# Kernel optimization log

Measured on AMD Instinct MI355X. Metric: run time of the kernel, lower is better.

Reference implementation:

```python
import jax, jax.numpy as jnp
import numpy as np

N = 50000
E = 800000
C = 64


def setup_inputs() -> dict:
    key = jax.random.key(0)
    ks = jax.random.split(key, 16)
    s = 0.05
    x = jax.random.normal(ks[0], (N, C), jnp.float32)
    edge_attr = jax.random.uniform(ks[1], (E, 4), dtype=jnp.float32)
    edge_index = jax.random.randint(ks[2], (2, E), 0, N)
    deg_hist = jax.random.uniform(ks[3], (N,), dtype=jnp.float32) * 32.0
    W = jax.random.normal(ks[4], (C, C), jnp.float32) * s          # self.weight[0]
    We = jax.random.normal(ks[5], (3, C), jnp.float32) * s         # edge_encoder
    be = jnp.zeros((C,), jnp.float32)
    Wpre = jax.random.normal(ks[6], (3 * C, C), jnp.float32) * s   # pre_nn Linear
    bpre = jnp.zeros((C,), jnp.float32)
    A_S = 4 * 3  # aggregators * scalers
    Wpost = jax.random.normal(ks[7], ((A_S + 1) * C, C), jnp.float32) * s
    bpost = jnp.zeros((C,), jnp.float32)
    Wih = jax.random.normal(ks[8], (C, 3 * C), jnp.float32) * s    # GRUCell input weights (transposed)
    bih = jnp.zeros((3 * C,), jnp.float32)
    Whh = jax.random.normal(ks[9], (C, 3 * C), jnp.float32) * s    # GRUCell hidden weights (transposed)
    bhh = jnp.zeros((3 * C,), jnp.float32)
    return dict(x=x, edge_attr=edge_attr, deg_hist=deg_hist, W=W, We=We, be=be,
                Wpre=Wpre, bpre=bpre, Wpost=Wpost, bpost=bpost,
                Wih=Wih, bih=bih, Whh=Whh, bhh=bhh, edge_index=edge_index)


def reference(x, edge_attr, deg_hist, W, We, be, Wpre, bpre, Wpost, bpost,
              Wih, bih, Whh, bhh, edge_index):
    n_nodes = x.shape[0]
    # gated path: m = x @ weight[0]
    m = x @ W  # [N, C]
    src, dst = edge_index[0], edge_index[1]
    # message: edge-weight scaling + edge encoder + pre-MLP (single Linear)
    ew = edge_attr[:, 3:4]                         # [E, 1]
    ea = edge_attr[:, :3] @ We + be                # [E, C]
    xi = ew * m[dst]                               # x_i (target)
    xj = ew * m[src]                               # x_j (source)
    ea = ew * ea
    h = jnp.concatenate([xi, xj, ea], axis=-1) @ Wpre + bpre  # [E, C]
    # multi-aggregator scatter: mean, min, max, std (keyed by target node)
    ones = jnp.ones((h.shape[0],), h.dtype)
    cnt = jax.ops.segment_sum(ones, dst, num_segments=n_nodes)       # [N]
    safe = jnp.maximum(cnt, 1.0)[:, None]
    s1 = jax.ops.segment_sum(h, dst, num_segments=n_nodes)
    s2 = jax.ops.segment_sum(h * h, dst, num_segments=n_nodes)
    mean = s1 / safe
    mean_sq = s2 / safe
    std = jnp.sqrt(jax.nn.relu(mean_sq - mean * mean) + 1e-5)
    has = (cnt > 0)[:, None]
    mn = jnp.where(has, jax.ops.segment_min(h, dst, num_segments=n_nodes), 0.0)
    mx = jnp.where(has, jax.ops.segment_max(h, dst, num_segments=n_nodes), 0.0)
    agg = jnp.concatenate([mean, mn, mx, std], axis=-1)  # [N, 4C]
    # degree scalers (faithfully replicating the cumulative reassignment in the torch loop)
    deg = jnp.maximum(cnt, 1.0)[:, None]
    avg_log = jnp.mean(jnp.log(deg_hist + 1.0))
    logd = jnp.log(deg + 1.0)
    o1 = agg                          # identity
    o2 = o1 * (logd / avg_log)        # amplification
    o3 = o2 * (avg_log / logd)        # attenuation applied on top of o2 (torch bug, kept)
    out = jnp.concatenate([o1, o2, o3], axis=-1)          # [N, 12C]
    # post-MLP on cat([m, aggregated])
    out = jnp.concatenate([m, out], axis=-1) @ Wpost + bpost  # [N, C]
    # GRUCell(out, x): torch gate order r, z, n
    gi = out @ Wih + bih
    gh = x @ Whh + bhh
    ir, iz, i_n = jnp.split(gi, 3, axis=-1)
    hr, hz, h_n = jnp.split(gh, 3, axis=-1)
    r = jax.nn.sigmoid(ir + hr)
    z = jax.nn.sigmoid(iz + hz)
    n = jnp.tanh(i_n + r * h_n)
    return (1.0 - z) * n + z * x
```

## Files before the change

### kernel.cpp

```cpp
#include <hip/hip_runtime.h>
#include <math.h>

#define NN  50000
#define NNP 50048
#define NE  800000
#define REP 16

#define B_BG1   0u
#define B_BG2A  49152u
#define B_BG2B  90112u
#define B_BG3   122880u
#define B_WE2   147456u
#define B_BE2   148224u
#define B_B3    148480u
#define B_SUML  149248u
#define B_XB    149504u
#define B_NF    6555648u
#define B_GH    19367936u
#define B_A2    38586368u
#define B_S2F   70617088u
#define B_CNT   70817280u
#define B_OFFS  74017280u
#define B_RANK  74217344u
#define B_ROFF  77417344u
#define B_EL2   80617344u
#define B_PART  87017344u

#define SCAN_B  196

typedef __attribute__((ext_vector_type(8))) short s8v;
typedef __attribute__((ext_vector_type(4))) short s4v;
typedef __attribute__((ext_vector_type(4))) float f4v;

__device__ inline short f2b(float f){
    union { float f; unsigned u; } v; v.f = f;
    unsigned r = v.u + 0x7fffu + ((v.u >> 16) & 1u);
    return (short)(r >> 16);
}
__device__ inline float b2f(short b){
    union { unsigned u; float f; } v; v.u = ((unsigned)(unsigned short)b) << 16;
    return v.f;
}

__global__ __launch_bounds__(256) void k_prep(const float* __restrict__ x,
    const float* __restrict__ dh, const int* __restrict__ dstA,
    const float* __restrict__ W, const float* __restrict__ Wpre,
    const float* __restrict__ We, const float* __restrict__ be,
    const float* __restrict__ bpost, const float* __restrict__ Wpost,
    const float* __restrict__ Wih, const float* __restrict__ bih,
    const float* __restrict__ Whh, int* __restrict__ cnt,
    int* __restrict__ rank, unsigned char* __restrict__ wsb)
{
    __shared__ float sred[4];
    int b = blockIdx.x, t = threadIdx.x;
    {
        int e = b * 256 + t;
        int r = b & (REP - 1);
        rank[e] = atomicAdd(&cnt[r * NN + dstA[e]], 1);
    }

    if (b < 38) {
        int idx = b * 256 + t;
        if (idx < 3072) {
            short* dst = (short*)(wsb + B_BG1);
            int lane = idx & 63, ts = idx >> 6;
            int tt = ts >> 1, s = ts & 1;
            int quad = lane >> 4, l15 = lane & 15, n = tt*16 + l15;
            for (int j = 0; j < 8; ++j) {
                int k = s*32 + quad*8 + j;
                float v;
                if (n < 64)       v = W[k*64 + n];
                else if (n < 128) { v = 0.f; for (int c = 0; c < 64; ++c) v += W[k*64+c]*Wpre[c*64 + (n-64)]; }
                else if (n < 192) { v = 0.f; for (int c = 0; c < 64; ++c) v += W[k*64+c]*Wpre[4096 + c*64 + (n-128)]; }
                else              v = Whh[k*192 + (n-192)];
                dst[((size_t)ts*64 + lane)*8 + j] = f2b(v);
            }
        } else if (idx < 5632) {
            int id = idx - 3072;
            short* dst = (short*)(wsb + B_BG2A);
            int lane = id & 63, ts = id >> 6;
            int quad = lane >> 4, l15 = lane & 15;
            int tt = ts / 10, s = ts % 10;
            int n = tt*16 + l15;
            for (int j = 0; j < 8; ++j) {
                int k = s*32 + quad*8 + j;
                float v;
                if (k < 64) v = Wpost[k*64 + n];
                else {
                    int kk = k - 64, ch = kk >> 2, st = kk & 3;
                    int ok = 64 + st*64 + ch;
                    v = Wpost[ok*64 + n] + Wpost[(ok + 512)*64 + n];
                }
                dst[((size_t)ts*64 + lane)*8 + j] = f2b(v);
            }
        } else if (idx < 7680) {
            int id = idx - 5632;
            short* dst = (short*)(wsb + B_BG2B);
            int lane = id & 63, ts = id >> 6;
            int quad = lane >> 4, l15 = lane & 15;
            int tt = ts / 8, s = ts % 8;
            int n = tt*16 + l15;
            for (int j = 0; j < 8; ++j) {
                int k = s*32 + quad*8 + j;
                int ch = k >> 2, st = k & 3;
                int ok = 320 + st*64 + ch;
                dst[((size_t)ts*64 + lane)*8 + j] = f2b(Wpost[ok*64 + n]);
            }
        } else if (idx < 9216) {
            int id = idx - 7680;
            short* dst = (short*)(wsb + B_BG3);
            int lane = id & 63, ts = id >> 6;
            int tt = ts >> 1, s = ts & 1;
            int quad = lane >> 4, l15 = lane & 15, n = tt*16 + l15;
            for (int j = 0; j < 8; ++j) {
                int k = s*32 + quad*8 + j;
                dst[((size_t)ts*64 + lane)*8 + j] = f2b(Wih[k*192 + n]);
            }
        } else if (idx < 9408) {
            int t2 = idx - 9216; int kk = t2 >> 6, j = t2 & 63;
            float v = 0.f;
            for (int c = 0; c < 64; ++c) v += We[kk*64 + c] * Wpre[(128+c)*64 + j];
            ((float*)(wsb + B_WE2))[t2] = v;
        } else if (idx < 9472) {
            int j = idx - 9408;
            float v = 0.f;
            for (int c = 0; c < 64; ++c) v += be[c] * Wpre[(128+c)*64 + j];
            ((float*)(wsb + B_BE2))[j] = v;
        } else if (idx < 9664) {
            int j = idx - 9472;
            float v = bih[j];
            for (int k = 0; k < 64; ++k) v += bpost[k] * Wih[k*192 + j];
            ((float*)(wsb + B_B3))[j] = v;
        }
    } else if (b < 1601) {
        int i = (b - 38) * 256 + t;
        if (i < 400000) {
            const float4* xp = (const float4*)(x + (size_t)i * 8);
            float4 p0 = xp[0], p1 = xp[1];
            s8v o;
            o[0]=f2b(p0.x); o[1]=f2b(p0.y); o[2]=f2b(p0.z); o[3]=f2b(p0.w);
            o[4]=f2b(p1.x); o[5]=f2b(p1.y); o[6]=f2b(p1.z); o[7]=f2b(p1.w);
            *(s8v*)((short*)(wsb + B_XB) + (size_t)i * 8) = o;
        }
    } else if (b < 1797) {
        int i = (b - 1601) * 256 + t;
        float v = (i < NN) ? logf(dh[i] + 1.f) : 0.f;
        #pragma unroll
        for (int m = 32; m >= 1; m >>= 1) v += __shfl_xor(v, m, 64);
        if ((t & 63) == 0) sred[t >> 6] = v;
        __syncthreads();
        if (t == 0) atomicAdd((float*)(wsb + B_SUML), sred[0]+sred[1]+sred[2]+sred[3]);
    }
}

__global__ __launch_bounds__(256) void k_scanA(const int* __restrict__ cnt,
    int* __restrict__ offs, int* __restrict__ roff, int* __restrict__ part)
{
    __shared__ int sh[256];
    int t = threadIdx.x, i = blockIdx.x * 256 + t;
    int v = 0;
    int pre[REP];
    if (i < NN) {
        #pragma unroll
        for (int r = 0; r < REP; ++r) {
            pre[r] = v;
            v += cnt[r * NN + i];
        }
    }
    sh[t] = v; __syncthreads();
    #pragma unroll
    for (int o = 1; o < 256; o <<= 1) {
        int u = (t >= o) ? sh[t - o] : 0;
        __syncthreads();
        sh[t] += u;
        __syncthreads();
    }
    if (i < NN) {
        offs[i] = sh[t] - v;
        int4* rp = (int4*)(roff + (size_t)i * REP);
        #pragma unroll
        for (int q = 0; q < REP/4; ++q)
            rp[q] = make_int4(pre[q*4], pre[q*4+1], pre[q*4+2], pre[q*4+3]);
    }
    if (t == 255) part[blockIdx.x] = sh[255];
}

__global__ __launch_bounds__(256) void k_scanC(const int* __restrict__ part,
    int* __restrict__ offs, int* __restrict__ roff)
{
    __shared__ int sh[256];
    int b = blockIdx.x, t = threadIdx.x;
    int v = (t < SCAN_B) ? part[t] : 0;
    sh[t] = v; __syncthreads();
    #pragma unroll
    for (int o = 1; o < 256; o <<= 1) {
        int u = (t >= o) ? sh[t - o] : 0;
        __syncthreads();
        sh[t] += u;
        __syncthreads();
    }
    int base = (b == 0) ? 0 : sh[b - 1];
    int i = b * 256 + t;
    if (i < NN) {
        int fo = offs[i] + base;
        offs[i] = fo;
        int4* rp = (int4*)(roff + (size_t)i * REP);
        #pragma unroll
        for (int q = 0; q < REP/4; ++q) {
            int4 r4 = rp[q];
            r4.x += fo; r4.y += fo; r4.z += fo; r4.w += fo;
            rp[q] = r4;
        }
    }
    if (b == 0 && t == 0) offs[NN] = NE;
}

__global__ __launch_bounds__(256) void k_scatter(const int* __restrict__ srcA,
    const int* __restrict__ dstA, const int* __restrict__ rank,
    const int* __restrict__ roff, int2* __restrict__ el2)
{
    int e = blockIdx.x * 256 + threadIdx.x;
    int r = blockIdx.x & (REP - 1);
    int dst = dstA[e];
    int p = roff[dst * REP + r] + rank[e];
    el2[p] = make_int2(e, srcA[e]);
}

__global__ __launch_bounds__(256) void k_g1(unsigned char* __restrict__ wsb)
{
    const short* xb = (const short*)(wsb + B_XB);
    const short* bf = (const short*)(wsb + B_BG1);
    short* a2 = (short*)(wsb + B_A2);
    short* nf = (short*)(wsb + B_NF);
    short* gh = (short*)(wsb + B_GH);
    int w = threadIdx.x >> 6, lane = threadIdx.x & 63;
    int quad = lane >> 4, l15 = lane & 15;
    int R0 = blockIdx.x * 64 + w * 16;
    const short* arow = xb + (size_t)(R0 + l15) * 64 + quad * 8;
    s8v a0 = *(const s8v*)(arow);
    s8v a1 = *(const s8v*)(arow + 32);
    f4v acc[24];
    #pragma unroll
    for (int t = 0; t < 24; ++t) acc[t] = (f4v){0.f,0.f,0.f,0.f};
    #pragma unroll
    for (int t = 0; t < 24; ++t) {
        s8v b0 = *(const s8v*)(bf + ((size_t)(t*2+0)*64 + lane)*8);
        s8v b1 = *(const s8v*)(bf + ((size_t)(t*2+1)*64 + lane)*8);
        acc[t] = __builtin_amdgcn_mfma_f32_16x16x32_bf16(a0, b0, acc[t], 0, 0, 0);
        acc[t] = __builtin_amdgcn_mfma_f32_16x16x32_bf16(a1, b1, acc[t], 0, 0, 0);
    }
    #pragma unroll
    for (int t = 0; t < 24; ++t) {
        #pragma unroll
        for (int r = 0; r < 4; ++r) {
            int row = R0 + quad*4 + r;
            if (row >= NN) continue;
            short v = f2b(acc[t][r]);
            if (t < 4)       a2[(size_t)row*320 + t*16 + l15] = v;
            else if (t < 12) nf[(size_t)row*128 + (t-4)*16 + l15] = v;
            else             gh[(size_t)row*192 + (t-12)*16 + l15] = v;
        }
    }
}

__global__ __launch_bounds__(256) void k_agg(const float* __restrict__ eattr,
    const float* __restrict__ bpre, unsigned char* __restrict__ wsb)
{
    __shared__ float4 sEA[4][64];
    __shared__ int    sOFF[4][64];
    int lane = threadIdx.x & 63;
    int w    = threadIdx.x >> 6;
    int wid  = blockIdx.x * 4 + w;
    const int* offs = (const int*)(wsb + B_OFFS);
    const int2* el2 = (const int2*)(wsb + B_EL2);
    const unsigned char* nfb = wsb + B_NF;
    const short* nf = (const short*)(wsb + B_NF);
    const float* we2p = (const float*)(wsb + B_WE2);
    float we0 = we2p[lane], we1 = we2p[64 + lane], we2v = we2p[128 + lane];
    float be2l = ((const float*)(wsb + B_BE2))[lane];
    float bprel = bpre[lane];
    float rcpavg = (float)NN / ((const float*)(wsb + B_SUML))[0];
    const float4* e4 = (const float4*)eattr;
    unsigned laneoff = 128u + 2u * (unsigned)lane;
    short* a2b = (short*)(wsb + B_A2);
    float* s2f = (float*)(wsb + B_S2F);

    for (int n = wid; n < NN; n += 8192) {
        float md2l = b2f(nf[(size_t)n * 128 + lane]);
        float tbase = md2l + be2l;
        int o0 = offs[n], o1e = offs[n + 1];
        float s = 0.f, ss = 0.f, mn = INFINITY, mx = -INFINITY;
        for (int base = o0; base < o1e; base += 64) {
            int cnt = o1e - base; if (cnt > 64) cnt = 64;
            if (lane < cnt) {
                int2 es = el2[base + lane];
                sOFF[w][lane] = es.y << 8;
                sEA[w][lane]  = e4[es.x];
            }
            for (int d0 = 0; d0 < cnt; d0 += 8) {
                float msv[8];
                #pragma unroll
                for (int u = 0; u < 8; ++u) {
                    int d = d0 + u; if (d > cnt - 1) d = cnt - 1;
                    unsigned off = (unsigned)sOFF[w][d] + laneoff;
                    msv[u] = b2f(*(const short*)(nfb + off));
                }
                #pragma unroll
                for (int u = 0; u < 8; ++u) {
                    int d = d0 + u;
                    if (d < cnt) {
                        float4 ea = sEA[w][d];
                        float t = tbase + msv[u];
                        t = fmaf(ea.x, we0, t);
                        t = fmaf(ea.y, we1, t);
                        t = fmaf(ea.z, we2v, t);
                        float h = fmaf(ea.w, t, bprel);
                        s += h; ss = fmaf(h, h, ss);
                        mn = fminf(mn, h); mx = fmaxf(mx, h);
                    }
                }
            }
        }
        int deg = o1e - o0;
        float safe = (float)(deg > 0 ? deg : 1);
        float mean = s / safe;
        float var  = ss / safe - mean * mean;
        float stdv = sqrtf(fmaxf(var, 0.f) + 1e-5f);
        if (deg == 0) { mn = 0.f; mx = 0.f; }
        s4v o; o[0] = f2b(mean); o[1] = f2b(mn); o[2] = f2b(mx); o[3] = f2b(stdv);
        *(s4v*)(a2b + (size_t)n * 320 + 64 + (lane << 2)) = o;
        if (lane == 0) s2f[n] = logf(safe + 1.f) * rcpavg;
    }
}

__global__ __launch_bounds__(256) void k_g23(const float* __restrict__ x,
    const float* __restrict__ bhh, unsigned char* __restrict__ wsb,
    float* __restrict__ out)
{
    __shared__ short sm[64 * 72];
    __shared__ float sS2[64];
    const short* a2  = (const short*)(wsb + B_A2);
    const short* bgA = (const short*)(wsb + B_BG2A);
    const short* bgB = (const short*)(wsb + B_BG2B);
    const short* bg3 = (const short*)(wsb + B_BG3);
    const short* gh  = (const short*)(wsb + B_GH);
    const float* b3  = (const float*)(wsb + B_B3);
    const float* s2f = (const float*)(wsb + B_S2F);
    int w = threadIdx.x >> 6, lane = threadIdx.x & 63;
    int quad = lane >> 4, l15 = lane & 15;
    int R0 = blockIdx.x * 64 + w * 16;

    {
        int i = threadIdx.x;
        if (i < 64) {
            int row = blockIdx.x * 64 + i;
            sS2[i] = (row < NN) ? s2f[row] : 0.f;
        }
    }

    const short* aBase = a2 + (size_t)(R0 + l15) * 320 + quad * 8;
    f4v acc1[4], acc2[4];
    #pragma unroll
    for (int t = 0; t < 4; ++t) { acc1[t] = (f4v){0.f,0.f,0.f,0.f}; acc2[t] = (f4v){0.f,0.f,0.f,0.f}; }
    #pragma unroll 2
    for (int s = 0; s < 10; ++s) {
        s8v a = *(const s8v*)(aBase + s * 32);
        #pragma unroll
        for (int t = 0; t < 4; ++t) {
            s8v b = *(const s8v*)(bgA + ((size_t)(t*10 + s)*64 + lane)*8);
            acc1[t] = __builtin_amdgcn_mfma_f32_16x16x32_bf16(a, b, acc1[t], 0, 0, 0);
        }
    }
    #pragma unroll 2
    for (int s = 0; s < 8; ++s) {
        s8v a = *(const s8v*)(aBase + 64 + s * 32);
        #pragma unroll
        for (int t = 0; t < 4; ++t) {
            s8v b = *(const s8v*)(bgB + ((size_t)(t*8 + s)*64 + lane)*8);
            acc2[t] = __builtin_amdgcn_mfma_f32_16x16x32_bf16(a, b, acc2[t], 0, 0, 0);
        }
    }
    __syncthreads();
    #pragma unroll
    for (int t = 0; t < 4; ++t)
        #pragma unroll
        for (int r = 0; r < 4; ++r) {
            int lr = w*16 + quad*4 + r;
            float v = acc1[t][r] + sS2[lr] * acc2[t][r];
            sm[lr * 72 + t*16 + l15] = f2b(v);
        }
    __syncthreads();

    const short* arow = sm + (w*16 + l15) * 72 + quad * 8;
    s8v a0 = *(const s8v*)(arow);
    s8v a1 = *(const s8v*)(arow + 32);
    f4v acc[12];
    #pragma unroll
    for (int t = 0; t < 12; ++t) acc[t] = (f4v){0.f,0.f,0.f,0.f};
    #pragma unroll
    for (int t = 0; t < 12; ++t) {
        s8v b0 = *(const s8v*)(bg3 + ((size_t)(t*2+0)*64 + lane)*8);
        s8v b1 = *(const s8v*)(bg3 + ((size_t)(t*2+1)*64 + lane)*8);
        acc[t] = __builtin_amdgcn_mfma_f32_16x16x32_bf16(a0, b0, acc[t], 0, 0, 0);
        acc[t] = __builtin_amdgcn_mfma_f32_16x16x32_bf16(a1, b1, acc[t], 0, 0, 0);
    }
    #pragma unroll
    for (int t = 0; t < 4; ++t) {
        #pragma unroll
        for (int r = 0; r < 4; ++r) {
            int row = R0 + quad*4 + r;
            if (row >= NN) continue;
            int c = t*16 + l15;
            float ir  = acc[t][r]   + b3[c];
            float iz  = acc[t+4][r] + b3[64 + c];
            float inn = acc[t+8][r] + b3[128 + c];
            const short* g = gh + (size_t)row * 192;
            float hr = b2f(g[c])       + bhh[c];
            float hz = b2f(g[64 + c])  + bhh[64 + c];
            float hn = b2f(g[128 + c]) + bhh[128 + c];
            float rr = 1.f / (1.f + expf(-(ir + hr)));
            float zz = 1.f / (1.f + expf(-(iz + hz)));
            float nn = tanhf(inn + rr * hn);
            out[(size_t)row*64 + c] = (1.f - zz)*nn + zz*x[(size_t)row*64 + c];
        }
    }
}

extern "C" void kernel_launch(void* const* d_in, const int* in_sizes, int n_in,
                              void* d_out, int out_size, void* d_ws, size_t ws_size,
                              hipStream_t stream)
{
    const float* x     = (const float*)d_in[0];
    const float* eattr = (const float*)d_in[1];
    const float* dh    = (const float*)d_in[2];
    const float* W     = (const float*)d_in[3];
    const float* We    = (const float*)d_in[4];
    const float* be    = (const float*)d_in[5];
    const float* Wpre  = (const float*)d_in[6];
    const float* bpre  = (const float*)d_in[7];
    const float* Wpost = (const float*)d_in[8];
    const float* bpost = (const float*)d_in[9];
    const float* Wih   = (const float*)d_in[10];
    const float* bih   = (const float*)d_in[11];
    const float* Whh   = (const float*)d_in[12];
    const float* bhh   = (const float*)d_in[13];
    const int*   eidx  = (const int*)d_in[14];
    unsigned char* wsb = (unsigned char*)d_ws;
    float* out = (float*)d_out;
    const int* srcA = eidx;
    const int* dstA = eidx + NE;
    int* cnt  = (int*)(wsb + B_CNT);
    int* offs = (int*)(wsb + B_OFFS);
    int* rank = (int*)(wsb + B_RANK);
    int* roff = (int*)(wsb + B_ROFF);
    int2* el2 = (int2*)(wsb + B_EL2);
    int* part = (int*)(wsb + B_PART);

    hipMemsetAsync(wsb + B_SUML, 0, 4, stream);
    hipMemsetAsync(cnt, 0, REP * NN * sizeof(int), stream);

    k_prep    <<<3125, 256, 0, stream>>>(x, dh, dstA, W, Wpre, We, be, bpost,
                                         Wpost, Wih, bih, Whh, cnt, rank, wsb);
    k_scanA   <<<SCAN_B, 256, 0, stream>>>(cnt, offs, roff, part);
    k_scanC   <<<SCAN_B, 256, 0, stream>>>(part, offs, roff);
    k_scatter <<<NE/256, 256, 0, stream>>>(srcA, dstA, rank, roff, el2);
    k_g1      <<<NNP/64, 256, 0, stream>>>(wsb);
    k_agg     <<<2048, 256, 0, stream>>>(eattr, bpre, wsb);
    k_g23     <<<NNP/64, 256, 0, stream>>>(x, bhh, wsb, out);
}
```

Baseline: 261.6 us.

## Fuse GRU hidden projection into final GEMM via stacked input/hidden weights

The x@Whh hidden-gate GEMM moves out of the first node GEMM, which no longer writes a bf16 gh buffer to workspace, and into the final kernel. There the GRU GEMM uses K=128 by concatenating the post-MLP output with bf16 x, with a block-structured weight that sums r/z contributions and keeps the n-gate hidden part separate. This removes the gh write and read (about 19 MB each way) and the per-element bias loads, at the cost of extra MFMAs, zero-padded weight blocks and more accumulator registers in k_g23.

New measurement: 310.0 us. +18.5%, slower.

```diff
diff --git a/kernel.cpp b/kernel.cpp
--- a/kernel.cpp
+++ b/kernel.cpp
@@ -7,24 +7,23 @@
 #define REP 16
 
 #define B_BG1   0u
-#define B_BG2A  49152u
-#define B_BG2B  90112u
-#define B_BG3   122880u
-#define B_WE2   147456u
-#define B_BE2   148224u
-#define B_B3    148480u
-#define B_SUML  149248u
-#define B_XB    149504u
-#define B_NF    6555648u
-#define B_GH    19367936u
-#define B_A2    38586368u
-#define B_S2F   70617088u
-#define B_CNT   70817280u
-#define B_OFFS  74017280u
-#define B_RANK  74217344u
-#define B_ROFF  77417344u
-#define B_EL2   80617344u
-#define B_PART  87017344u
+#define B_BG2A  24576u
+#define B_BG2B  65536u
+#define B_BG3   98304u
+#define B_WE2   163840u
+#define B_BE2   164608u
+#define B_B4    164864u
+#define B_SUML  165888u
+#define B_XB    166912u
+#define B_NF    6573056u
+#define B_A2    19385344u
+#define B_S2F   51416064u
+#define B_CNT   51616064u
+#define B_OFFS  54816064u
+#define B_RANK  55016072u
+#define B_ROFF  58216072u
+#define B_EL2   61416072u
+#define B_PART  67816072u
 
 #define SCAN_B  196
 
@@ -48,8 +47,9 @@
     const float* __restrict__ We, const float* __restrict__ be,
     const float* __restrict__ bpost, const float* __restrict__ Wpost,
     const float* __restrict__ Wih, const float* __restrict__ bih,
-    const float* __restrict__ Whh, int* __restrict__ cnt,
-    int* __restrict__ rank, unsigned char* __restrict__ wsb)
+    const float* __restrict__ Whh, const float* __restrict__ bhh,
+    int* __restrict__ cnt, int* __restrict__ rank,
+    unsigned char* __restrict__ wsb)
 {
     __shared__ float sred[4];
     int b = blockIdx.x, t = threadIdx.x;
@@ -59,27 +59,27 @@
         rank[e] = atomicAdd(&cnt[r * NN + dstA[e]], 1);
     }
 
-    if (b < 38) {
+    if (b < 42) {
         int idx = b * 256 + t;
-        if (idx < 3072) {
+        int lane = idx & 63;
+        int quad = lane >> 4, l15 = lane & 15;
+        if (idx < 1536) {
             short* dst = (short*)(wsb + B_BG1);
-            int lane = idx & 63, ts = idx >> 6;
+            int ts = idx >> 6;
             int tt = ts >> 1, s = ts & 1;
-            int quad = lane >> 4, l15 = lane & 15, n = tt*16 + l15;
+            int n = tt*16 + l15;
             for (int j = 0; j < 8; ++j) {
                 int k = s*32 + quad*8 + j;
                 float v;
                 if (n < 64)       v = W[k*64 + n];
                 else if (n < 128) { v = 0.f; for (int c = 0; c < 64; ++c) v += W[k*64+c]*Wpre[c*64 + (n-64)]; }
-                else if (n < 192) { v = 0.f; for (int c = 0; c < 64; ++c) v += W[k*64+c]*Wpre[4096 + c*64 + (n-128)]; }
-                else              v = Whh[k*192 + (n-192)];
+                else              { v = 0.f; for (int c = 0; c < 64; ++c) v += W[k*64+c]*Wpre[4096 + c*64 + (n-128)]; }
                 dst[((size_t)ts*64 + lane)*8 + j] = f2b(v);
             }
-        } else if (idx < 5632) {
-            int id = idx - 3072;
+        } else if (idx < 4096) {
+            int id = idx - 1536;
             short* dst = (short*)(wsb + B_BG2A);
-            int lane = id & 63, ts = id >> 6;
-            int quad = lane >> 4, l15 = lane & 15;
+            int ts = id >> 6;
             int tt = ts / 10, s = ts % 10;
             int n = tt*16 + l15;
             for (int j = 0; j < 8; ++j) {
@@ -93,11 +93,10 @@
                 }
                 dst[((size_t)ts*64 + lane)*8 + j] = f2b(v);
             }
-        } else if (idx < 7680) {
-            int id = idx - 5632;
+        } else if (idx < 6144) {
+            int id = idx - 4096;
             short* dst = (short*)(wsb + B_BG2B);
-            int lane = id & 63, ts = id >> 6;
-            int quad = lane >> 4, l15 = lane & 15;
+            int ts = id >> 6;
             int tt = ts / 8, s = ts % 8;
             int n = tt*16 + l15;
             for (int j = 0; j < 8; ++j) {
@@ -106,34 +105,46 @@
                 int ok = 320 + st*64 + ch;
                 dst[((size_t)ts*64 + lane)*8 + j] = f2b(Wpost[ok*64 + n]);
             }
-        } else if (idx < 9216) {
-            int id = idx - 7680;
+        } else if (idx < 10240) {
+            int id = idx - 6144;
             short* dst = (short*)(wsb + B_BG3);
-            int lane = id & 63, ts = id >> 6;
-            int tt = ts >> 1, s = ts & 1;
-            int quad = lane >> 4, l15 = lane & 15, n = tt*16 + l15;
+            int ts = id >> 6;
+            int tt = ts >> 2, s = ts & 3;
+            int n = tt*16 + l15;
             for (int j = 0; j < 8; ++j) {
                 int k = s*32 + quad*8 + j;
-                dst[((size_t)ts*64 + lane)*8 + j] = f2b(Wih[k*192 + n]);
-            }
-        } else if (idx < 9408) {
-            int t2 = idx - 9216; int kk = t2 >> 6, j = t2 & 63;
+                float v;
+                if (k < 64) v = (n < 192) ? Wih[k*192 + n] : 0.f;
+                else {
+                    int kk = k - 64;
+                    if (n < 128)      v = Whh[kk*192 + n];
+                    else if (n < 192) v = 0.f;
+                    else              v = Whh[kk*192 + 128 + (n - 192)];
+                }
+                dst[((size_t)ts*64 + lane)*8 + j] = f2b(v);
+            }
+        } else if (idx < 10432) {
+            int t2 = idx - 10240; int kk = t2 >> 6, j = t2 & 63;
             float v = 0.f;
             for (int c = 0; c < 64; ++c) v += We[kk*64 + c] * Wpre[(128+c)*64 + j];
             ((float*)(wsb + B_WE2))[t2] = v;
-        } else if (idx < 9472) {
-            int j = idx - 9408;
+        } else if (idx < 10496) {
+            int j = idx - 10432;
             float v = 0.f;
             for (int c = 0; c < 64; ++c) v += be[c] * Wpre[(128+c)*64 + j];
             ((float*)(wsb + B_BE2))[j] = v;
-        } else if (idx < 9664) {
-            int j = idx - 9472;
-            float v = bih[j];
-            for (int k = 0; k < 64; ++k) v += bpost[k] * Wih[k*192 + j];
-            ((float*)(wsb + B_B3))[j] = v;
-        }
-    } else if (b < 1601) {
-        int i = (b - 38) * 256 + t;
+        } else if (idx < 10752) {
+            int j = idx - 10496;
+            float v;
+            if (j < 192) {
+                v = bih[j];
+                for (int k = 0; k < 64; ++k) v += bpost[k] * Wih[k*192 + j];
+                if (j < 128) v += bhh[j];
+            } else v = bhh[128 + (j - 192)];
+            ((float*)(wsb + B_B4))[j] = v;
+        }
+    } else if (b < 1605) {
+        int i = (b - 42) * 256 + t;
         if (i < 400000) {
             const float4* xp = (const float4*)(x + (size_t)i * 8);
             float4 p0 = xp[0], p1 = xp[1];
@@ -142,8 +153,8 @@
             o[4]=f2b(p1.x); o[5]=f2b(p1.y); o[6]=f2b(p1.z); o[7]=f2b(p1.w);
             *(s8v*)((short*)(wsb + B_XB) + (size_t)i * 8) = o;
         }
-    } else if (b < 1797) {
-        int i = (b - 1601) * 256 + t;
+    } else if (b < 1801) {
+        int i = (b - 1605) * 256 + t;
         float v = (i < NN) ? logf(dh[i] + 1.f) : 0.f;
         #pragma unroll
         for (int m = 32; m >= 1; m >>= 1) v += __shfl_xor(v, m, 64);
@@ -162,10 +173,7 @@
     int pre[REP];
     if (i < NN) {
         #pragma unroll
-        for (int r = 0; r < REP; ++r) {
-            pre[r] = v;
-            v += cnt[r * NN + i];
-        }
+        for (int r = 0; r < REP; ++r) { pre[r] = v; v += cnt[r * NN + i]; }
     }
     sh[t] = v; __syncthreads();
     #pragma unroll
@@ -232,33 +240,31 @@
     const short* bf = (const short*)(wsb + B_BG1);
     short* a2 = (short*)(wsb + B_A2);
     short* nf = (short*)(wsb + B_NF);
-    short* gh = (short*)(wsb + B_GH);
     int w = threadIdx.x >> 6, lane = threadIdx.x & 63;
     int quad = lane >> 4, l15 = lane & 15;
     int R0 = blockIdx.x * 64 + w * 16;
     const short* arow = xb + (size_t)(R0 + l15) * 64 + quad * 8;
     s8v a0 = *(const s8v*)(arow);
     s8v a1 = *(const s8v*)(arow + 32);
-    f4v acc[24];
-    #pragma unroll
-    for (int t = 0; t < 24; ++t) acc[t] = (f4v){0.f,0.f,0.f,0.f};
-    #pragma unroll
-    for (int t = 0; t < 24; ++t) {
+    f4v acc[12];
+    #pragma unroll
+    for (int t = 0; t < 12; ++t) acc[t] = (f4v){0.f,0.f,0.f,0.f};
+    #pragma unroll
+    for (int t = 0; t < 12; ++t) {
         s8v b0 = *(const s8v*)(bf + ((size_t)(t*2+0)*64 + lane)*8);
         s8v b1 = *(const s8v*)(bf + ((size_t)(t*2+1)*64 + lane)*8);
         acc[t] = __builtin_amdgcn_mfma_f32_16x16x32_bf16(a0, b0, acc[t], 0, 0, 0);
         acc[t] = __builtin_amdgcn_mfma_f32_16x16x32_bf16(a1, b1, acc[t], 0, 0, 0);
     }
     #pragma unroll
-    for (int t = 0; t < 24; ++t) {
+    for (int t = 0; t < 12; ++t) {
         #pragma unroll
         for (int r = 0; r < 4; ++r) {
             int row = R0 + quad*4 + r;
             if (row >= NN) continue;
             short v = f2b(acc[t][r]);
-            if (t < 4)       a2[(size_t)row*320 + t*16 + l15] = v;
-            else if (t < 12) nf[(size_t)row*128 + (t-4)*16 + l15] = v;
-            else             gh[(size_t)row*192 + (t-12)*16 + l15] = v;
+            if (t < 4) a2[(size_t)row*320 + t*16 + l15] = v;
+            else       nf[(size_t)row*128 + (t-4)*16 + l15] = v;
         }
     }
 }
@@ -334,21 +340,24 @@
 }
 
 __global__ __launch_bounds__(256) void k_g23(const float* __restrict__ x,
-    const float* __restrict__ bhh, unsigned char* __restrict__ wsb,
-    float* __restrict__ out)
+    unsigned char* __restrict__ wsb, float* __restrict__ out)
 {
     __shared__ short sm[64 * 72];
     __shared__ float sS2[64];
     const short* a2  = (const short*)(wsb + B_A2);
+    const short* xb  = (const short*)(wsb + B_XB);
     const short* bgA = (const short*)(wsb + B_BG2A);
     const short* bgB = (const short*)(wsb + B_BG2B);
     const short* bg3 = (const short*)(wsb + B_BG3);
-    const short* gh  = (const short*)(wsb + B_GH);
-    const float* b3  = (const float*)(wsb + B_B3);
+    const float* b4  = (const float*)(wsb + B_B4);
     const float* s2f = (const float*)(wsb + B_S2F);
     int w = threadIdx.x >> 6, lane = threadIdx.x & 63;
     int quad = lane >> 4, l15 = lane & 15;
     int R0 = blockIdx.x * 64 + w * 16;
+
+    const short* xrow = xb + (size_t)(R0 + l15) * 64 + quad * 8;
+    s8v q0 = *(const s8v*)(xrow);
+    s8v q1 = *(const s8v*)(xrow + 32);
 
     {
         int i = threadIdx.x;
@@ -392,17 +401,21 @@
     __syncthreads();
 
     const short* arow = sm + (w*16 + l15) * 72 + quad * 8;
-    s8v a0 = *(const s8v*)(arow);
-    s8v a1 = *(const s8v*)(arow + 32);
-    f4v acc[12];
-    #pragma unroll
-    for (int t = 0; t < 12; ++t) acc[t] = (f4v){0.f,0.f,0.f,0.f};
-    #pragma unroll
-    for (int t = 0; t < 12; ++t) {
-        s8v b0 = *(const s8v*)(bg3 + ((size_t)(t*2+0)*64 + lane)*8);
-        s8v b1 = *(const s8v*)(bg3 + ((size_t)(t*2+1)*64 + lane)*8);
-        acc[t] = __builtin_amdgcn_mfma_f32_16x16x32_bf16(a0, b0, acc[t], 0, 0, 0);
-        acc[t] = __builtin_amdgcn_mfma_f32_16x16x32_bf16(a1, b1, acc[t], 0, 0, 0);
+    s8v p0 = *(const s8v*)(arow);
+    s8v p1 = *(const s8v*)(arow + 32);
+    f4v acc[16];
+    #pragma unroll
+    for (int t = 0; t < 16; ++t) acc[t] = (f4v){0.f,0.f,0.f,0.f};
+    #pragma unroll 4
+    for (int t = 0; t < 16; ++t) {
+        s8v b0 = *(const s8v*)(bg3 + ((size_t)(t*4+0)*64 + lane)*8);
+        s8v b1 = *(const s8v*)(bg3 + ((size_t)(t*4+1)*64 + lane)*8);
+        s8v b2 = *(const s8v*)(bg3 + ((size_t)(t*4+2)*64 + lane)*8);
+        s8v b3v= *(const s8v*)(bg3 + ((size_t)(t*4+3)*64 + lane)*8);
+        acc[t] = __builtin_amdgcn_mfma_f32_16x16x32_bf16(p0, b0, acc[t], 0, 0, 0);
+        acc[t] = __builtin_amdgcn_mfma_f32_16x16x32_bf16(p1, b1, acc[t], 0, 0, 0);
+        acc[t] = __builtin_amdgcn_mfma_f32_16x16x32_bf16(q0, b2, acc[t], 0, 0, 0);
+        acc[t] = __builtin_amdgcn_mfma_f32_16x16x32_bf16(q1, b3v, acc[t], 0, 0, 0);
     }
     #pragma unroll
     for (int t = 0; t < 4; ++t) {
@@ -411,16 +424,13 @@
             int row = R0 + quad*4 + r;
             if (row >= NN) continue;
             int c = t*16 + l15;
-            float ir  = acc[t][r]   + b3[c];
-            float iz  = acc[t+4][r] + b3[64 + c];
-            float inn = acc[t+8][r] + b3[128 + c];
-            const short* g = gh + (size_t)row * 192;
-            float hr = b2f(g[c])       + bhh[c];
-            float hz = b2f(g[64 + c])  + bhh[64 + c];
-            float hn = b2f(g[128 + c]) + bhh[128 + c];
-            float rr = 1.f / (1.f + expf(-(ir + hr)));
-            float zz = 1.f / (1.f + expf(-(iz + hz)));
-            float nn = tanhf(inn + rr * hn);
+            float srz = acc[t][r]    + b4[c];
+            float szz = acc[t+4][r]  + b4[64 + c];
+            float inn = acc[t+8][r]  + b4[128 + c];
+            float hnn = acc[t+12][r] + b4[192 + c];
+            float rr = 1.f / (1.f + expf(-srz));
+            float zz = 1.f / (1.f + expf(-szz));
+            float nn = tanhf(fmaf(rr, hnn, inn));
             out[(size_t)row*64 + c] = (1.f - zz)*nn + zz*x[(size_t)row*64 + c];
         }
     }
@@ -460,11 +470,11 @@
     hipMemsetAsync(cnt, 0, REP * NN * sizeof(int), stream);
 
     k_prep    <<<3125, 256, 0, stream>>>(x, dh, dstA, W, Wpre, We, be, bpost,
-                                         Wpost, Wih, bih, Whh, cnt, rank, wsb);
+                                         Wpost, Wih, bih, Whh, bhh, cnt, rank, wsb);
     k_scanA   <<<SCAN_B, 256, 0, stream>>>(cnt, offs, roff, part);
     k_scanC   <<<SCAN_B, 256, 0, stream>>>(part, offs, roff);
     k_scatter <<<NE/256, 256, 0, stream>>>(srcA, dstA, rank, roff, el2);
     k_g1      <<<NNP/64, 256, 0, stream>>>(wsb);
     k_agg     <<<2048, 256, 0, stream>>>(eattr, bpre, wsb);
-    k_g23     <<<NNP/64, 256, 0, stream>>>(x, bhh, wsb, out);
-}
+    k_g23     <<<NNP/64, 256, 0, stream>>>(x, wsb, out);
+}
```
